# Kernel optimization log

Hardware: AMD Instinct MI355X
Metric: run time of the kernel (lower is better)

## Reference

```python
import jax, jax.numpy as jnp
import numpy as np
from jax import lax

VOCAB, EMBED, CELL, LABELS = 32000, 128, 256, 128
B, T = 64, 256
N_LAYERS = 8


def _lstm_layer(x, mask, Wi, Wh, b, reverse):
    """Keras-semantics masked LSTM. x:[B,T,D], mask:[B,T] bool.
    If reverse (go_backwards=True): process reversed seq and return the
    REVERSED output sequence (Keras does NOT flip it back).
    Masked steps: carry h,c and emit previous h (Keras rnn mask behavior).
    Gate order i,f,c,o as in Keras kernels."""
    if reverse:
        x = x[:, ::-1]
        mask = mask[:, ::-1]
    Bs = x.shape[0]
    H = Wh.shape[0]
    xW = jnp.einsum('btd,dg->btg', x, Wi) + b  # [B,T,4H] precomputed input proj

    def step(carry, inp):
        h, c = carry
        g, m = inp  # g:[B,4H], m:[B]
        z = g + h @ Wh
        i, f, cb, o = jnp.split(z, 4, axis=-1)
        i = jax.nn.sigmoid(i)
        f = jax.nn.sigmoid(f)
        o = jax.nn.sigmoid(o)
        c_new = f * c + i * jnp.tanh(cb)
        h_new = o * jnp.tanh(c_new)
        m_ = m[:, None]
        h = jnp.where(m_, h_new, h)
        c = jnp.where(m_, c_new, c)
        return (h, c), h

    h0 = jnp.zeros((Bs, H), x.dtype)
    _, ys = lax.scan(step, (h0, h0), (xW.transpose(1, 0, 2), mask.T))
    return ys.transpose(1, 0, 2)  # [B,T,H], in processing order (no re-flip)


def setup_inputs() -> dict:
    key = jax.random.key(0)
    ks = jax.random.split(key, 9)
    word_ids = jax.random.randint(ks[0], (B, T), 0, VOCAB, dtype=jnp.int32)
    predicate_ids = jax.random.randint(ks[1], (B, T), 0, 2, dtype=jnp.int32)
    emb1 = jax.random.normal(ks[2], (VOCAB, EMBED), jnp.float32) * 0.1
    # binary feature embedding init: row0 zeros, row1 ones (as in source)
    emb2 = jnp.vstack([jnp.zeros((1, EMBED)), jnp.ones((1, EMBED))]).astype(jnp.float32)
    s = 0.05
    Wis = jax.random.normal(ks[3], (N_LAYERS, CELL, 4 * CELL), jnp.float32) * s  # layer0 in-dim 2*EMBED==CELL
    Whs = jax.random.normal(ks[4], (N_LAYERS, CELL, 4 * CELL), jnp.float32) * s
    bs = jnp.zeros((N_LAYERS, 4 * CELL), jnp.float32)
    bs = bs.at[:, CELL:2 * CELL].set(1.0)  # unit_forget_bias
    Wd = jax.random.normal(ks[5], (CELL, LABELS), jnp.float32) * s
    bd = jnp.zeros((LABELS,), jnp.float32)
    return {'word_ids': word_ids, 'predicate_ids': predicate_ids,
            'emb1': emb1, 'emb2': emb2, 'Wis': Wis, 'Whs': Whs, 'bs': bs,
            'Wd': Wd, 'bd': bd}


def reference(word_ids, predicate_ids, emb1, emb2, Wis, Whs, bs, Wd, bd):
    mask = word_ids != 0  # mask_zero semantics of embedding1
    encoded0 = jnp.concatenate([emb1[word_ids], emb2[predicate_ids]], axis=2)  # [B,T,2E]
    outs = []
    for i in range(N_LAYERS):
        if i == 0:
            inp = encoded0
        elif i == 1:
            inp = outs[0]
        else:
            inp = outs[i - 2] + outs[i - 1]
        outs.append(_lstm_layer(inp, mask, Wis[i], Whs[i], bs[i], reverse=(i % 2 == 1)))
    encoded_2d = (outs[6] + outs[7]).reshape(-1, CELL)  # [B*T, CELL]
    return jax.nn.softmax(encoded_2d @ Wd + bd, axis=-1)
```

## Files before the change

### kernel.cpp

```cpp
#include <hip/hip_runtime.h>


typedef _Float16 f16;
typedef _Float16 f16x8 __attribute__((ext_vector_type(8)));
typedef _Float16 f16x4 __attribute__((ext_vector_type(4)));
typedef float    f32x4 __attribute__((ext_vector_type(4)));

#define DEVI static __device__ __forceinline__

DEVI float fast_sigmoid(float x) {
  return __builtin_amdgcn_rcpf(1.f + __builtin_amdgcn_exp2f(-1.44269504f * x));
}
DEVI float fast_tanh(float x) {
  return 1.f - 2.f * __builtin_amdgcn_rcpf(1.f + __builtin_amdgcn_exp2f(2.88539008f * x));
}
DEVI int ntg_of(int w, int j2) { return ((j2 >> 1) << 4) + 2 * w + (j2 & 1); }

__global__ void pack_frags(const float* __restrict__ src, f16* __restrict__ dst, int nct) {
  const int idx  = blockIdx.x * 256 + threadIdx.x;
  const int lane = idx & 63;
  const int f    = idx >> 6;
  const int nt   = f % nct;
  const int g2   = f / nct;
  const int kk   = g2 & 7;
  const int L    = g2 >> 3;
  const int ncols = nct * 16;
  const float* s = src + (size_t)(L * 256 + kk * 32 + (lane >> 4) * 8) * ncols + nt * 16 + (lane & 15);
  f16x8 v;
#pragma unroll
  for (int e = 0; e < 8; ++e) v[e] = (f16)s[(size_t)e * ncols];
  *(f16x8*)(dst + (size_t)idx * 8) = v;
}

__global__ void embed_k(const int* __restrict__ wid, const int* __restrict__ pid,
                        const float* __restrict__ emb1, const float* __restrict__ emb2,
                        f16* __restrict__ X) {
  const int r = blockIdx.x;
  const int d = threadIdx.x;
  const int wv = wid[r], pv = pid[r];
  X[r * 256 + d]       = (f16)emb1[wv * 128 + d];
  X[r * 256 + 128 + d] = (f16)emb2[pv * 128 + d];
}

__global__ void make_input(const float* __restrict__ a, const float* __restrict__ b,
                           f16* __restrict__ X, int two) {
  const int q = blockIdx.x * 256 + threadIdx.x;
  float4 v = ((const float4*)a)[q];
  if (two) {
    float4 u = ((const float4*)b)[q];
    v.x += u.x; v.y += u.y; v.z += u.z; v.w += u.w;
  }
  f16x4 h; h[0] = (f16)v.x; h[1] = (f16)v.y; h[2] = (f16)v.z; h[3] = (f16)v.w;
  *(f16x4*)(X + (size_t)q * 4) = h;
}

__global__ __launch_bounds__(512, 2) void gemm_xw(const f16* __restrict__ X,
                                                  const f16* __restrict__ wipf,
                                                  const float* __restrict__ bias,
                                                  f16* __restrict__ xW) {
  extern __shared__ char smem[];
  const int tid = threadIdx.x, lane = tid & 63, w = tid >> 6;
  const int nb = blockIdx.x, mb = blockIdx.y;
  const char* xbase = (const char*)X + (size_t)mb * 128 * 512;
#pragma unroll
  for (int i = 0; i < 8; ++i) {
    const int row = i * 16 + (tid >> 5);
    const int c16 = tid & 31;
    const uint4 v = *(const uint4*)(xbase + row * 512 + c16 * 16);
    *(uint4*)(smem + row * 512 + ((c16 ^ (row & 7)) << 4)) = v;
  }
  __syncthreads();

  const int mh = w >> 2, nw = w & 3;
  const char* wipf_c = (const char*)wipf;
  const float vb0 = bias[nb * 128 + nw * 32 + (lane & 15)];
  const float vb1 = bias[nb * 128 + nw * 32 + 16 + (lane & 15)];
  f32x4 acc[4][2] = {};
#pragma unroll
  for (int kk = 0; kk < 8; ++kk) {
    const f16x8 b0 = *(const f16x8*)(wipf_c + ((size_t)(kk * 64 + nb * 8 + nw * 2 + 0) << 10) + (lane << 4));
    const f16x8 b1 = *(const f16x8*)(wipf_c + ((size_t)(kk * 64 + nb * 8 + nw * 2 + 1) << 10) + (lane << 4));
#pragma unroll
    for (int m2 = 0; m2 < 4; ++m2) {
      const int row = mh * 64 + m2 * 16 + (lane & 15);
      const f16x8 a = *(const f16x8*)(smem + row * 512 + (((kk * 4 + (lane >> 4)) ^ (row & 7)) << 4));
      acc[m2][0] = __builtin_amdgcn_mfma_f32_16x16x32_f16(a, b0, acc[m2][0], 0, 0, 0);
      acc[m2][1] = __builtin_amdgcn_mfma_f32_16x16x32_f16(a, b1, acc[m2][1], 0, 0, 0);
    }
  }
#pragma unroll
  for (int m2 = 0; m2 < 4; ++m2)
#pragma unroll
    for (int n2 = 0; n2 < 2; ++n2)
#pragma unroll
      for (int j = 0; j < 4; ++j) {
        const int r  = mb * 128 + mh * 64 + m2 * 16 + (lane >> 4) * 4 + j;
        const int cc = nb * 128 + nw * 32 + n2 * 16 + (lane & 15);
        xW[(size_t)r * 1024 + cc] = (f16)(acc[m2][n2][j] + (n2 ? vb1 : vb0));
      }
}

__global__ __launch_bounds__(512, 2) void lstm_layer(
    const f16*  __restrict__ xW,
    const int*  __restrict__ wid,
    const f16*  __restrict__ whp,
    float* __restrict__ out,
    int reverse) {
  extern __shared__ char smem[];
  f16* hbuf = (f16*)(smem + 131072);
  const int tid  = threadIdx.x;
  const int lane = tid & 63, w = tid >> 6;
  const int g    = blockIdx.x;
  const int r0   = lane & 15;
  const int rg   = lane >> 4;
  const int ct0  = 2 * w;
  const char* whp_c = (const char*)whp;

  {
    const char* src = whp_c + (4 << 16);
#pragma unroll
    for (int i = 0; i < 16; ++i) {
      const int off = i * 8192 + tid * 16;
      *(uint4*)(smem + off) = *(const uint4*)(src + off);
    }
  }
  for (int i = tid; i < 2 * 16 * 264; i += 512) hbuf[i] = (f16)0.f;

  f16x8 regB[32];
#pragma unroll
  for (int kk = 0; kk < 4; ++kk)
#pragma unroll
    for (int j2 = 0; j2 < 8; ++j2)
      regB[kk * 8 + j2] = *(const f16x8*)(whp_c + ((size_t)(kk * 64 + ntg_of(w, j2)) << 10) + (lane << 4));

  float c[8], hreg[8];
#pragma unroll
  for (int i = 0; i < 8; ++i) { c[i] = 0.f; hreg[i] = 0.f; }

  __syncthreads();

#pragma unroll 1
  for (int k = 0; k < 256; ++k) {
    const int t_in = reverse ? (255 - k) : k;
    const f16* hc = hbuf + (k & 1) * 4224;
    f16*       hn = hbuf + ((k & 1) ^ 1) * 4224;

    f16 xwv[32];
    int widv[4];
#pragma unroll
    for (int j = 0; j < 4; ++j) {
      const int b   = g * 16 + rg * 4 + j;
      const int row = (b << 8) + t_in;
      widv[j] = wid[row];
#pragma unroll
      for (int j2 = 0; j2 < 8; ++j2)
        xwv[j2 * 4 + j] = xW[(size_t)row * 1024 + ntg_of(w, j2) * 16 + r0];
    }

    f16x8 sb6[8];
#pragma unroll
    for (int j2 = 0; j2 < 8; ++j2)
      sb6[j2] = *(const f16x8*)(whp_c + ((size_t)(6 * 64 + ntg_of(w, j2)) << 10) + (lane << 4));

    f32x4 acc[8] = {};
    f16x8 af[8];
#pragma unroll
    for (int kk = 0; kk < 4; ++kk) {
      af[kk] = *(const f16x8*)&hc[r0 * 264 + kk * 32 + rg * 8];
#pragma unroll
      for (int j2 = 0; j2 < 8; ++j2)
        acc[j2] = __builtin_amdgcn_mfma_f32_16x16x32_f16(af[kk], regB[kk * 8 + j2], acc[j2], 0, 0, 0);
    }

    af[6] = *(const f16x8*)&hc[r0 * 264 + 6 * 32 + rg * 8];
#pragma unroll
    for (int j2 = 0; j2 < 8; ++j2)
      acc[j2] = __builtin_amdgcn_mfma_f32_16x16x32_f16(af[6], sb6[j2], acc[j2], 0, 0, 0);

    __builtin_amdgcn_sched_barrier(0x30F);
    f16x8 sb7[8];
#pragma unroll
    for (int j2 = 0; j2 < 8; ++j2)
      sb7[j2] = *(const f16x8*)(whp_c + ((size_t)(7 * 64 + ntg_of(w, j2)) << 10) + (lane << 4));

#pragma unroll
    for (int kk = 4; kk < 6; ++kk) {
      af[kk] = *(const f16x8*)&hc[r0 * 264 + kk * 32 + rg * 8];
#pragma unroll
      for (int j2 = 0; j2 < 8; ++j2) {
        const f16x8 b8 = *(const f16x8*)(smem + ((size_t)((kk - 4) * 64 + ntg_of(w, j2)) << 10) + (lane << 4));
        acc[j2] = __builtin_amdgcn_mfma_f32_16x16x32_f16(af[kk], b8, acc[j2], 0, 0, 0);
      }
    }

    af[7] = *(const f16x8*)&hc[r0 * 264 + 7 * 32 + rg * 8];
#pragma unroll
    for (int j2 = 0; j2 < 8; ++j2)
      acc[j2] = __builtin_amdgcn_mfma_f32_16x16x32_f16(af[7], sb7[j2], acc[j2], 0, 0, 0);

#pragma unroll
    for (int p = 0; p < 2; ++p) {
#pragma unroll
      for (int j = 0; j < 4; ++j) {
        const int idx = p * 4 + j;
        const float zi = acc[p    ][j] + (float)xwv[(p    ) * 4 + j];
        const float zf = acc[2 + p][j] + (float)xwv[(2 + p) * 4 + j];
        const float zc = acc[4 + p][j] + (float)xwv[(4 + p) * 4 + j];
        const float zo = acc[6 + p][j] + (float)xwv[(6 + p) * 4 + j];
        const float ig = fast_sigmoid(zi);
        const float fg = fast_sigmoid(zf);
        const float og = fast_sigmoid(zo);
        const float cb = fast_tanh(zc);
        const float cn = fg * c[idx] + ig * cb;
        const float hn_ = og * fast_tanh(cn);
        const bool  m  = (widv[j] != 0);
        c[idx] = m ? cn : c[idx];
        const float hv = m ? hn_ : hreg[idx];
        hreg[idx] = hv;
        const int b = g * 16 + rg * 4 + j;
        out[(size_t)(((b << 8) + k) << 8) + (ct0 + p) * 16 + r0] = hv;
      }
    }

#pragma unroll
    for (int p = 0; p < 2; ++p)
#pragma unroll
      for (int j = 0; j < 4; ++j)
        hn[(rg * 4 + j) * 264 + (ct0 + p) * 16 + r0] = (f16)hreg[p * 4 + j];

    __builtin_amdgcn_sched_barrier(0);
    asm volatile("s_waitcnt lgkmcnt(0)\n\ts_barrier" ::: "memory");
    __builtin_amdgcn_sched_barrier(0);
  }
}

__global__ __launch_bounds__(512, 2) void final_k(const float* __restrict__ o0,
                                                  const float* __restrict__ o1,
                                                  const f16* __restrict__ wdpf,
                                                  const float* __restrict__ bd,
                                                  float* __restrict__ outp) {
  const int tid = threadIdx.x, lane = tid & 63, w = tid >> 6;
  const int rbase = blockIdx.x * 128 + w * 16;
  const char* wdpf_c = (const char*)wdpf;

  f32x4 acc[8] = {};
#pragma unroll
  for (int kk = 0; kk < 8; ++kk) {
    const int r  = rbase + (lane & 15);
    const int k0 = kk * 32 + (lane >> 4) * 8;
    const float4* p0 = (const float4*)(o0 + (size_t)r * 256 + k0);
    const float4* p1 = (const float4*)(o1 + (size_t)r * 256 + k0);
    const float4 x0 = p0[0], x1 = p0[1], y0 = p1[0], y1 = p1[1];
    f16x8 a;
    a[0] = (f16)(x0.x + y0.x); a[1] = (f16)(x0.y + y0.y);
    a[2] = (f16)(x0.z + y0.z); a[3] = (f16)(x0.w + y0.w);
    a[4] = (f16)(x1.x + y1.x); a[5] = (f16)(x1.y + y1.y);
    a[6] = (f16)(x1.z + y1.z); a[7] = (f16)(x1.w + y1.w);
#pragma unroll
    for (int nt = 0; nt < 8; ++nt) {
      const f16x8 b = *(const f16x8*)(wdpf_c + ((size_t)(kk * 8 + nt) << 10) + (lane << 4));
      acc[nt] = __builtin_amdgcn_mfma_f32_16x16x32_f16(a, b, acc[nt], 0, 0, 0);
    }
  }

  float vb[8];
#pragma unroll
  for (int nt = 0; nt < 8; ++nt) vb[nt] = bd[nt * 16 + (lane & 15)];

#pragma unroll
  for (int j = 0; j < 4; ++j) {
    float v[8];
#pragma unroll
    for (int nt = 0; nt < 8; ++nt) v[nt] = acc[nt][j] + vb[nt];
    float mx = v[0];
#pragma unroll
    for (int nt = 1; nt < 8; ++nt) mx = fmaxf(mx, v[nt]);
#pragma unroll
    for (int m = 1; m < 16; m <<= 1) mx = fmaxf(mx, __shfl_xor(mx, m, 64));
    float s = 0.f;
#pragma unroll
    for (int nt = 0; nt < 8; ++nt) {
      v[nt] = __builtin_amdgcn_exp2f(1.44269504f * (v[nt] - mx));
      s += v[nt];
    }
#pragma unroll
    for (int m = 1; m < 16; m <<= 1) s += __shfl_xor(s, m, 64);
    const float rs = __builtin_amdgcn_rcpf(s);
    const int r = rbase + (lane >> 4) * 4 + j;
#pragma unroll
    for (int nt = 0; nt < 8; ++nt)
      outp[(size_t)r * 128 + nt * 16 + (lane & 15)] = v[nt] * rs;
  }
}

extern "C" void kernel_launch(void* const* d_in, const int* in_sizes, int n_in,
                              void* d_out, int out_size, void* d_ws, size_t ws_size,
                              hipStream_t stream) {
  const int*   wid  = (const int*)d_in[0];
  const int*   pid  = (const int*)d_in[1];
  const float* emb1 = (const float*)d_in[2];
  const float* emb2 = (const float*)d_in[3];
  const float* Wis  = (const float*)d_in[4];
  const float* Whs  = (const float*)d_in[5];
  const float* bs   = (const float*)d_in[6];
  const float* Wd   = (const float*)d_in[7];
  const float* bd   = (const float*)d_in[8];

  char* ws = (char*)d_ws;
  f16*   Whp  = (f16*)(ws + 0);
  f16*   Wipf = (f16*)(ws + 4194304);
  f16*   Wdpf = (f16*)(ws + 8388608);
  f16*   X    = (f16*)(ws + 8454144);
  f16*   xW   = (f16*)(ws + 16842752);
  float* o0   = (float*)(ws + 50397184);
  float* o1   = (float*)(ws + 67174400);

  hipFuncSetAttribute((const void*)lstm_layer, hipFuncAttributeMaxDynamicSharedMemorySize, 147968);
  hipFuncSetAttribute((const void*)gemm_xw,    hipFuncAttributeMaxDynamicSharedMemorySize, 65536);

  pack_frags<<<1024, 256, 0, stream>>>(Whs, Whp, 64);
  pack_frags<<<1024, 256, 0, stream>>>(Wis, Wipf, 64);
  pack_frags<<<16,   256, 0, stream>>>(Wd,  Wdpf, 8);
  embed_k<<<16384, 128, 0, stream>>>(wid, pid, emb1, emb2, X);

  float* obuf[2] = {o0, o1};
  for (int L = 0; L < 8; ++L) {
    if (L == 1)
      make_input<<<4096, 256, 0, stream>>>(o0, o0, X, 0);
    else if (L >= 2)
      make_input<<<4096, 256, 0, stream>>>(obuf[L & 1], obuf[(L - 1) & 1], X, 1);
    gemm_xw<<<dim3(8, 128), 512, 65536, stream>>>(X, Wipf + (size_t)L * 262144, bs + L * 1024, xW);
    lstm_layer<<<4, 512, 147968, stream>>>(xW, wid, Whp + (size_t)L * 262144, obuf[L & 1], L & 1);
  }
  final_k<<<128, 512, 0, stream>>>(o0, o1, Wdpf, bd, (float*)d_out);
}
```

Baseline: 11.95 ms.

## Interleave xW gate layout, prefetch next step, store LSTM outputs as fp16

The gemm writes xW with the four gates of each hidden unit interleaved, so the LSTM step can fetch them with one 8-byte load per unit. The next timestep's values are prefetched during the current step's MFMAs. The word mask is precomputed once into a shared-memory bitmask instead of reading word ids every step. Layer outputs are stored as fp16, which halves output traffic, lets layer 1 read them directly with no conversion kernel, and simplifies make_input and final_k. In exchange, the residual sums are now done in fp16, which adds rounding error.

Result: no change. 12.12 ms (+1.4%).

```diff
diff --git a/kernel.cpp b/kernel.cpp
--- a/kernel.cpp
+++ b/kernel.cpp
@@ -42,22 +42,18 @@
   X[r * 256 + 128 + d] = (f16)emb2[pv * 128 + d];
 }
 
-__global__ void make_input(const float* __restrict__ a, const float* __restrict__ b,
-                           f16* __restrict__ X, int two) {
-  const int q = blockIdx.x * 256 + threadIdx.x;
-  float4 v = ((const float4*)a)[q];
-  if (two) {
-    float4 u = ((const float4*)b)[q];
-    v.x += u.x; v.y += u.y; v.z += u.z; v.w += u.w;
-  }
-  f16x4 h; h[0] = (f16)v.x; h[1] = (f16)v.y; h[2] = (f16)v.z; h[3] = (f16)v.w;
-  *(f16x4*)(X + (size_t)q * 4) = h;
+__global__ void make_input(const f16* __restrict__ a, const f16* __restrict__ b,
+                           f16* __restrict__ X) {
+  const size_t q = ((size_t)blockIdx.x * 256 + threadIdx.x) * 8;
+  const f16x8 va = *(const f16x8*)(a + q);
+  const f16x8 vb = *(const f16x8*)(b + q);
+  *(f16x8*)(X + q) = va + vb;
 }
 
 __global__ __launch_bounds__(512, 2) void gemm_xw(const f16* __restrict__ X,
                                                   const f16* __restrict__ wipf,
                                                   const float* __restrict__ bias,
-                                                  f16* __restrict__ xW) {
+                                                  f16* __restrict__ xWp) {
   extern __shared__ char smem[];
   const int tid = threadIdx.x, lane = tid & 63, w = tid >> 6;
   const int nb = blockIdx.x, mb = blockIdx.y;
@@ -94,25 +90,26 @@
     for (int n2 = 0; n2 < 2; ++n2)
 #pragma unroll
       for (int j = 0; j < 4; ++j) {
-        const int r  = mb * 128 + mh * 64 + m2 * 16 + (lane >> 4) * 4 + j;
-        const int cc = nb * 128 + nw * 32 + n2 * 16 + (lane & 15);
-        xW[(size_t)r * 1024 + cc] = (f16)(acc[m2][n2][j] + (n2 ? vb1 : vb0));
+        const int r   = mb * 128 + mh * 64 + m2 * 16 + (lane >> 4) * 4 + j;
+        const int col = nb * 128 + nw * 32 + n2 * 16 + (lane & 15);
+        xWp[(size_t)r * 1024 + (col & 255) * 4 + (col >> 8)] =
+            (f16)(acc[m2][n2][j] + (n2 ? vb1 : vb0));
       }
 }
 
 __global__ __launch_bounds__(512, 2) void lstm_layer(
-    const f16*  __restrict__ xW,
+    const f16*  __restrict__ xWp,
     const int*  __restrict__ wid,
     const f16*  __restrict__ whp,
-    float* __restrict__ out,
+    f16* __restrict__ out,
     int reverse) {
   extern __shared__ char smem[];
-  f16* hbuf = (f16*)(smem + 131072);
+  f16*      hbuf   = (f16*)(smem + 131072);
+  unsigned* mask16 = (unsigned*)(smem + 147968);
   const int tid  = threadIdx.x;
   const int lane = tid & 63, w = tid >> 6;
   const int g    = blockIdx.x;
-  const int r0   = lane & 15;
-  const int rg   = lane >> 4;
+  const int r0   = lane & 15, rg = lane >> 4;
   const int ct0  = 2 * w;
   const char* whp_c = (const char*)whp;
 
@@ -125,6 +122,13 @@
     }
   }
   for (int i = tid; i < 2 * 16 * 264; i += 512) hbuf[i] = (f16)0.f;
+  if (tid < 256) {
+    unsigned m = 0;
+#pragma unroll
+    for (int j = 0; j < 16; ++j)
+      m |= (wid[((g * 16 + j) << 8) + tid] != 0) ? (1u << j) : 0u;
+    mask16[tid] = m;
+  }
 
   f16x8 regB[32];
 #pragma unroll
@@ -136,6 +140,15 @@
   float c[8], hreg[8];
 #pragma unroll
   for (int i = 0; i < 8; ++i) { c[i] = 0.f; hreg[i] = 0.f; }
+
+  const int t0 = reverse ? 255 : 0;
+  f16x4 xwc[2][4];
+#pragma unroll
+  for (int p = 0; p < 2; ++p)
+#pragma unroll
+    for (int j = 0; j < 4; ++j)
+      xwc[p][j] = *(const f16x4*)(xWp + (size_t)(((g * 16 + rg * 4 + j) << 8) + t0) * 1024
+                                  + ((ct0 + p) * 16 + r0) * 4);
 
   __syncthreads();
 
@@ -145,97 +158,97 @@
     const f16* hc = hbuf + (k & 1) * 4224;
     f16*       hn = hbuf + ((k & 1) ^ 1) * 4224;
 
-    f16 xwv[32];
-    int widv[4];
-#pragma unroll
-    for (int j = 0; j < 4; ++j) {
-      const int b   = g * 16 + rg * 4 + j;
-      const int row = (b << 8) + t_in;
-      widv[j] = wid[row];
-#pragma unroll
-      for (int j2 = 0; j2 < 8; ++j2)
-        xwv[j2 * 4 + j] = xW[(size_t)row * 1024 + ntg_of(w, j2) * 16 + r0];
-    }
-
-    f16x8 sb6[8];
+    f16x8 sb6[8], sb7[8];
 #pragma unroll
     for (int j2 = 0; j2 < 8; ++j2)
       sb6[j2] = *(const f16x8*)(whp_c + ((size_t)(6 * 64 + ntg_of(w, j2)) << 10) + (lane << 4));
-
-    f32x4 acc[8] = {};
-    f16x8 af[8];
-#pragma unroll
-    for (int kk = 0; kk < 4; ++kk) {
-      af[kk] = *(const f16x8*)&hc[r0 * 264 + kk * 32 + rg * 8];
-#pragma unroll
-      for (int j2 = 0; j2 < 8; ++j2)
-        acc[j2] = __builtin_amdgcn_mfma_f32_16x16x32_f16(af[kk], regB[kk * 8 + j2], acc[j2], 0, 0, 0);
-    }
-
-    af[6] = *(const f16x8*)&hc[r0 * 264 + 6 * 32 + rg * 8];
-#pragma unroll
-    for (int j2 = 0; j2 < 8; ++j2)
-      acc[j2] = __builtin_amdgcn_mfma_f32_16x16x32_f16(af[6], sb6[j2], acc[j2], 0, 0, 0);
-
-    __builtin_amdgcn_sched_barrier(0x30F);
-    f16x8 sb7[8];
 #pragma unroll
     for (int j2 = 0; j2 < 8; ++j2)
       sb7[j2] = *(const f16x8*)(whp_c + ((size_t)(7 * 64 + ntg_of(w, j2)) << 10) + (lane << 4));
 
+    f32x4 acc[8] = {};
+#pragma unroll
+    for (int kk = 0; kk < 4; ++kk) {
+      const f16x8 a = *(const f16x8*)&hc[r0 * 264 + kk * 32 + rg * 8];
+#pragma unroll
+      for (int j2 = 0; j2 < 8; ++j2)
+        acc[j2] = __builtin_amdgcn_mfma_f32_16x16x32_f16(a, regB[kk * 8 + j2], acc[j2], 0, 0, 0);
+    }
+
 #pragma unroll
     for (int kk = 4; kk < 6; ++kk) {
-      af[kk] = *(const f16x8*)&hc[r0 * 264 + kk * 32 + rg * 8];
+      const f16x8 a = *(const f16x8*)&hc[r0 * 264 + kk * 32 + rg * 8];
 #pragma unroll
       for (int j2 = 0; j2 < 8; ++j2) {
         const f16x8 b8 = *(const f16x8*)(smem + ((size_t)((kk - 4) * 64 + ntg_of(w, j2)) << 10) + (lane << 4));
-        acc[j2] = __builtin_amdgcn_mfma_f32_16x16x32_f16(af[kk], b8, acc[j2], 0, 0, 0);
+        acc[j2] = __builtin_amdgcn_mfma_f32_16x16x32_f16(a, b8, acc[j2], 0, 0, 0);
       }
     }
 
-    af[7] = *(const f16x8*)&hc[r0 * 264 + 7 * 32 + rg * 8];
-#pragma unroll
-    for (int j2 = 0; j2 < 8; ++j2)
-      acc[j2] = __builtin_amdgcn_mfma_f32_16x16x32_f16(af[7], sb7[j2], acc[j2], 0, 0, 0);
-
+    {
+      const f16x8 a6 = *(const f16x8*)&hc[r0 * 264 + 6 * 32 + rg * 8];
+#pragma unroll
+      for (int j2 = 0; j2 < 8; ++j2)
+        acc[j2] = __builtin_amdgcn_mfma_f32_16x16x32_f16(a6, sb6[j2], acc[j2], 0, 0, 0);
+      const f16x8 a7 = *(const f16x8*)&hc[r0 * 264 + 7 * 32 + rg * 8];
+#pragma unroll
+      for (int j2 = 0; j2 < 8; ++j2)
+        acc[j2] = __builtin_amdgcn_mfma_f32_16x16x32_f16(a7, sb7[j2], acc[j2], 0, 0, 0);
+    }
+
+    const int tn = (k < 255) ? (reverse ? 254 - k : k + 1) : t0;
+    f16x4 xwn[2][4];
+#pragma unroll
+    for (int p = 0; p < 2; ++p)
+#pragma unroll
+      for (int j = 0; j < 4; ++j)
+        xwn[p][j] = *(const f16x4*)(xWp + (size_t)(((g * 16 + rg * 4 + j) << 8) + tn) * 1024
+                                    + ((ct0 + p) * 16 + r0) * 4);
+
+    const unsigned mw = mask16[t_in];
 #pragma unroll
     for (int p = 0; p < 2; ++p) {
 #pragma unroll
       for (int j = 0; j < 4; ++j) {
         const int idx = p * 4 + j;
-        const float zi = acc[p    ][j] + (float)xwv[(p    ) * 4 + j];
-        const float zf = acc[2 + p][j] + (float)xwv[(2 + p) * 4 + j];
-        const float zc = acc[4 + p][j] + (float)xwv[(4 + p) * 4 + j];
-        const float zo = acc[6 + p][j] + (float)xwv[(6 + p) * 4 + j];
+        const float zi = acc[0 + p][j] + (float)xwc[p][j][0];
+        const float zf = acc[2 + p][j] + (float)xwc[p][j][1];
+        const float zc = acc[4 + p][j] + (float)xwc[p][j][2];
+        const float zo = acc[6 + p][j] + (float)xwc[p][j][3];
         const float ig = fast_sigmoid(zi);
         const float fg = fast_sigmoid(zf);
         const float og = fast_sigmoid(zo);
         const float cb = fast_tanh(zc);
         const float cn = fg * c[idx] + ig * cb;
-        const float hn_ = og * fast_tanh(cn);
-        const bool  m  = (widv[j] != 0);
-        c[idx] = m ? cn : c[idx];
-        const float hv = m ? hn_ : hreg[idx];
-        hreg[idx] = hv;
-        const int b = g * 16 + rg * 4 + j;
-        out[(size_t)(((b << 8) + k) << 8) + (ct0 + p) * 16 + r0] = hv;
+        const float hv_ = og * fast_tanh(cn);
+        const bool  m  = ((mw >> (rg * 4 + j)) & 1u) != 0u;
+        c[idx]    = m ? cn : c[idx];
+        hreg[idx] = m ? hv_ : hreg[idx];
       }
     }
 
 #pragma unroll
     for (int p = 0; p < 2; ++p)
 #pragma unroll
-      for (int j = 0; j < 4; ++j)
-        hn[(rg * 4 + j) * 264 + (ct0 + p) * 16 + r0] = (f16)hreg[p * 4 + j];
+      for (int j = 0; j < 4; ++j) {
+        const f16 hv = (f16)hreg[p * 4 + j];
+        hn[(rg * 4 + j) * 264 + (ct0 + p) * 16 + r0] = hv;
+        out[((size_t)((g * 16 + rg * 4 + j) << 8) + k) * 256 + (ct0 + p) * 16 + r0] = hv;
+      }
 
     __builtin_amdgcn_sched_barrier(0);
     asm volatile("s_waitcnt lgkmcnt(0)\n\ts_barrier" ::: "memory");
     __builtin_amdgcn_sched_barrier(0);
-  }
-}
-
-__global__ __launch_bounds__(512, 2) void final_k(const float* __restrict__ o0,
-                                                  const float* __restrict__ o1,
+
+#pragma unroll
+    for (int p = 0; p < 2; ++p)
+#pragma unroll
+      for (int j = 0; j < 4; ++j) xwc[p][j] = xwn[p][j];
+  }
+}
+
+__global__ __launch_bounds__(512, 2) void final_k(const f16* __restrict__ o0,
+                                                  const f16* __restrict__ o1,
                                                   const f16* __restrict__ wdpf,
                                                   const float* __restrict__ bd,
                                                   float* __restrict__ outp) {
@@ -248,14 +261,9 @@
   for (int kk = 0; kk < 8; ++kk) {
     const int r  = rbase + (lane & 15);
     const int k0 = kk * 32 + (lane >> 4) * 8;
-    const float4* p0 = (const float4*)(o0 + (size_t)r * 256 + k0);
-    const float4* p1 = (const float4*)(o1 + (size_t)r * 256 + k0);
-    const float4 x0 = p0[0], x1 = p0[1], y0 = p1[0], y1 = p1[1];
-    f16x8 a;
-    a[0] = (f16)(x0.x + y0.x); a[1] = (f16)(x0.y + y0.y);
-    a[2] = (f16)(x0.z + y0.z); a[3] = (f16)(x0.w + y0.w);
-    a[4] = (f16)(x1.x + y1.x); a[5] = (f16)(x1.y + y1.y);
-    a[6] = (f16)(x1.z + y1.z); a[7] = (f16)(x1.w + y1.w);
+    const f16x8 x = *(const f16x8*)(o0 + (size_t)r * 256 + k0);
+    const f16x8 y = *(const f16x8*)(o1 + (size_t)r * 256 + k0);
+    const f16x8 a = x + y;
 #pragma unroll
     for (int nt = 0; nt < 8; ++nt) {
       const f16x8 b = *(const f16x8*)(wdpf_c + ((size_t)(kk * 8 + nt) << 10) + (lane << 4));
@@ -307,30 +315,34 @@
   const float* bd   = (const float*)d_in[8];
 
   char* ws = (char*)d_ws;
-  f16*   Whp  = (f16*)(ws + 0);
-  f16*   Wipf = (f16*)(ws + 4194304);
-  f16*   Wdpf = (f16*)(ws + 8388608);
-  f16*   X    = (f16*)(ws + 8454144);
-  f16*   xW   = (f16*)(ws + 16842752);
-  float* o0   = (float*)(ws + 50397184);
-  float* o1   = (float*)(ws + 67174400);
-
-  hipFuncSetAttribute((const void*)lstm_layer, hipFuncAttributeMaxDynamicSharedMemorySize, 147968);
+  f16* Whp  = (f16*)(ws + 0);
+  f16* Wipf = (f16*)(ws + 4194304);
+  f16* Wdpf = (f16*)(ws + 8388608);
+  f16* X    = (f16*)(ws + 8454144);
+  f16* xWp  = (f16*)(ws + 16842752);
+  f16* o0   = (f16*)(ws + 50397184);
+  f16* o1   = (f16*)(ws + 58785792);
+
   hipFuncSetAttribute((const void*)gemm_xw,    hipFuncAttributeMaxDynamicSharedMemorySize, 65536);
+  hipFuncSetAttribute((const void*)lstm_layer, hipFuncAttributeMaxDynamicSharedMemorySize, 148992);
 
   pack_frags<<<1024, 256, 0, stream>>>(Whs, Whp, 64);
   pack_frags<<<1024, 256, 0, stream>>>(Wis, Wipf, 64);
   pack_frags<<<16,   256, 0, stream>>>(Wd,  Wdpf, 8);
   embed_k<<<16384, 128, 0, stream>>>(wid, pid, emb1, emb2, X);
 
-  float* obuf[2] = {o0, o1};
+  f16* obuf[2] = {o0, o1};
   for (int L = 0; L < 8; ++L) {
-    if (L == 1)
-      make_input<<<4096, 256, 0, stream>>>(o0, o0, X, 0);
-    else if (L >= 2)
-      make_input<<<4096, 256, 0, stream>>>(obuf[L & 1], obuf[(L - 1) & 1], X, 1);
-    gemm_xw<<<dim3(8, 128), 512, 65536, stream>>>(X, Wipf + (size_t)L * 262144, bs + L * 1024, xW);
-    lstm_layer<<<4, 512, 147968, stream>>>(xW, wid, Whp + (size_t)L * 262144, obuf[L & 1], L & 1);
+    const f16* xin = X;
+    if (L == 1) {
+      xin = o0;
+    } else if (L >= 2) {
+      make_input<<<2048, 256, 0, stream>>>(obuf[L & 1], obuf[(L - 1) & 1], X);
+    }
+    gemm_xw<<<dim3(8, 128), 512, 65536, stream>>>(xin, Wipf + (size_t)L * 262144,
+                                                  bs + L * 1024, xWp);
+    lstm_layer<<<4, 512, 148992, stream>>>(xWp, wid, Whp + (size_t)L * 262144,
+                                           obuf[L & 1], L & 1);
   }
   final_k<<<128, 512, 0, stream>>>(o0, o1, Wdpf, bd, (float*)d_out);
 }
```
